# Kernel optimization log

Hardware: AMD Instinct MI355X
Metric: run time of the kernel (lower is better)

Reference implementation:

```python
import jax, jax.numpy as jnp
import numpy as np

# Hyperparameters (from init_kwargs)
D_MODEL = 1024
D_STATE = 64
HEADDIM = 64
MIMO_RANK = 2
CHUNK = 128
EXPAND = 2
D_INNER = EXPAND * D_MODEL            # 2048
NHEADS = D_INNER // HEADDIM           # 32
G = MIMO_RANK * D_STATE               # effective state channels per head = 128
D_CONV = 4
D_XBC = D_INNER + 2 * NHEADS * G      # conv channels
D_IN_PROJ = 2 * D_INNER + 2 * NHEADS * G + NHEADS  # [z, x, B, C, dt]


def rmsnorm(x, w, eps=1e-5):
    return x * w * jax.lax.rsqrt(jnp.mean(x * x, axis=-1, keepdims=True) + eps)


def setup_inputs() -> dict:
    key = jax.random.key(0)
    ks = jax.random.split(key, 8)
    B, L = 2, 2048
    x = jax.random.normal(ks[0], (B, L, D_MODEL), jnp.float32)
    norm_w = jnp.ones((D_MODEL,), jnp.float32)
    in_proj_w = jax.random.normal(ks[1], (D_IN_PROJ, D_MODEL), jnp.float32) * 0.02
    conv_w = jax.random.normal(ks[2], (D_XBC, D_CONV), jnp.float32) * 0.2
    conv_b = jnp.zeros((D_XBC,), jnp.float32)
    dt_bias = jax.random.uniform(ks[3], (NHEADS,), jnp.float32, minval=-4.0, maxval=-1.0)
    A_log = jnp.log(jax.random.uniform(ks[4], (NHEADS,), jnp.float32, minval=1.0, maxval=8.0))
    D_skip = jnp.ones((NHEADS,), jnp.float32)
    gnorm_w = jnp.ones((D_INNER,), jnp.float32)
    out_proj_w = jax.random.normal(ks[5], (D_MODEL, D_INNER), jnp.float32) * 0.02
    return dict(x=x, norm_w=norm_w, in_proj_w=in_proj_w, conv_w=conv_w, conv_b=conv_b,
                dt_bias=dt_bias, A_log=A_log, D_skip=D_skip, gnorm_w=gnorm_w,
                out_proj_w=out_proj_w)


def _mamba3(u, in_proj_w, conv_w, conv_b, dt_bias, A_log, D_skip, gnorm_w, out_proj_w):
    B, L, _ = u.shape
    H, P = NHEADS, HEADDIM
    nc = L // CHUNK

    zxbcdt = u @ in_proj_w.T                                   # (B,L,D_IN_PROJ)
    z, xbc, dt_raw = jnp.split(zxbcdt, [D_INNER, D_INNER + D_XBC], axis=-1)

    # causal depthwise conv (width D_CONV) + SiLU on [x, B, C]
    xp = jnp.pad(xbc, ((0, 0), (D_CONV - 1, 0), (0, 0)))
    conv = conv_b + sum(xp[:, k:k + L, :] * conv_w[:, k] for k in range(D_CONV))
    xbc = jax.nn.silu(conv)
    xh, Bm, Cm = jnp.split(xbc, [D_INNER, D_INNER + H * G], axis=-1)

    Xc = xh.reshape(B, nc, CHUNK, H, P)
    Bc = Bm.reshape(B, nc, CHUNK, H, G)
    Cc = Cm.reshape(B, nc, CHUNK, H, G)

    dt = jax.nn.softplus(dt_raw + dt_bias)                     # (B,L,H), positive
    A = -jnp.exp(A_log)                                        # (H,), negative
    dtc = dt.reshape(B, nc, CHUNK, H)
    a = dtc * A                                                # log decay, (B,nc,cs,H)
    cum = jnp.cumsum(a, axis=2)                                # inclusive cumsum within chunk

    # intra-chunk (quadratic, causal) part
    cumT = cum.transpose(0, 1, 3, 2)                           # (B,nc,H,cs)
    diff = cumT[..., :, None] - cumT[..., None, :]             # cum_l - cum_s
    mask = jnp.tril(jnp.ones((CHUNK, CHUNK), bool))
    decay = jnp.where(mask, jnp.exp(jnp.where(mask, diff, 0.0)), 0.0)
    dtT = dtc.transpose(0, 1, 3, 2)                            # (B,nc,H,cs)
    scores = jnp.einsum('bclhg,bcshg->bchls', Cc, Bc) * decay * dtT[:, :, :, None, :]
    Y_intra = jnp.einsum('bchls,bcshp->bclhp', scores, Xc)

    # inter-chunk state recurrence
    w = jnp.exp(cum[:, :, -1:, :] - cum) * dtc                 # (B,nc,cs,H)
    S = jnp.einsum('bcshg,bcshp->bchgp', Bc * w[..., None], Xc)  # chunk states
    dlast = jnp.exp(cum[:, :, -1, :])                          # (B,nc,H) total chunk decay

    def step(carry, inp):
        dl, s = inp
        return dl[:, :, None, None] * carry + s, carry

    init = jnp.zeros((B, H, G, P), u.dtype)
    _, Hprev = jax.lax.scan(step, init, (dlast.transpose(1, 0, 2), S.transpose(1, 0, 2, 3, 4)))
    Hprev = Hprev.transpose(1, 0, 2, 3, 4)                     # (B,nc,H,G,P) state before chunk
    Y_inter = jnp.einsum('bclhg,bchgp->bclhp', Cc * jnp.exp(cum)[..., None], Hprev)

    y = (Y_intra + Y_inter + D_skip[:, None] * Xc).reshape(B, L, D_INNER)
    y = rmsnorm(y * jax.nn.silu(z), gnorm_w)                   # gated RMSNorm
    return y @ out_proj_w.T


def reference(x, norm_w, in_proj_w, conv_w, conv_b, dt_bias, A_log, D_skip, gnorm_w, out_proj_w):
    # pre-norm residual wrapper
    return x + _mamba3(rmsnorm(x, norm_w), in_proj_w, conv_w, conv_b,
                       dt_bias, A_log, D_skip, gnorm_w, out_proj_w)
```

## Files before the change

kernel.cpp:

```cpp
#include <hip/hip_runtime.h>

typedef unsigned short u16;
typedef __attribute__((ext_vector_type(8))) short bf16x8;
typedef __attribute__((ext_vector_type(4))) float f32x4;

#define MFMA16(a,b,c) __builtin_amdgcn_mfma_f32_16x16x32_bf16(a,b,c,0,0,0)

#define DMODEL   1024
#define DINNER   2048
#define NHEADS   32
#define HEADDIM  64
#define GDIM     128
#define DXBC     10240
#define DPROJ    12320
#define CHUNK_L  128
#define NCHUNK   16
#define NROWS    4096

__device__ __forceinline__ float b2f(u16 u){ return __uint_as_float(((unsigned)u)<<16); }
__device__ __forceinline__ u16 f2b(float f){
  unsigned u = __float_as_uint(f);
  u += 0x7fffu + ((u>>16)&1u);
  return (u16)(u>>16);
}

__device__ __forceinline__ void gload_lds16(const void* g, void* l){
  __builtin_amdgcn_global_load_lds(
      (const __attribute__((address_space(1))) unsigned int*)g,
      (__attribute__((address_space(3))) unsigned int*)l, 16, 0, 0);
}

__global__ void k_f32_to_bf16(const float* __restrict__ src, u16* __restrict__ dst, int n){
  int i = blockIdx.x*blockDim.x + threadIdx.x;
  int stride = gridDim.x*blockDim.x;
  int n4 = n >> 2;
  for (int j=i; j<n4; j+=stride){
    float4 v = reinterpret_cast<const float4*>(src)[j];
    uint2 o;
    o.x = (unsigned)f2b(v.x) | ((unsigned)f2b(v.y)<<16);
    o.y = (unsigned)f2b(v.z) | ((unsigned)f2b(v.w)<<16);
    reinterpret_cast<uint2*>(dst)[j] = o;
  }
}

__global__ __launch_bounds__(256) void k_rmsnorm_in(const float* __restrict__ x,
                                                    const float* __restrict__ w,
                                                    u16* __restrict__ u){
  int row = blockIdx.x, tid = threadIdx.x;
  float4 v = reinterpret_cast<const float4*>(x + (size_t)row*DMODEL)[tid];
  float ss = v.x*v.x + v.y*v.y + v.z*v.z + v.w*v.w;
  #pragma unroll
  for (int off=32; off>0; off>>=1) ss += __shfl_down(ss, off, 64);
  __shared__ float red[4];
  if ((tid&63)==0) red[tid>>6] = ss;
  __syncthreads();
  float tot = red[0]+red[1]+red[2]+red[3];
  float sc = rsqrtf(tot/(float)DMODEL + 1e-5f);
  float4 wv = reinterpret_cast<const float4*>(w)[tid];
  uint2 o;
  o.x = (unsigned)f2b(v.x*wv.x*sc) | ((unsigned)f2b(v.y*wv.y*sc)<<16);
  o.y = (unsigned)f2b(v.z*wv.z*sc) | ((unsigned)f2b(v.w*wv.w*sc)<<16);
  reinterpret_cast<uint2*>(u + (size_t)row*DMODEL)[tid] = o;
}

__global__ __launch_bounds__(512) void k_gemm1_p2(const u16* __restrict__ A,
                                                  const u16* __restrict__ W,
                                                  u16* __restrict__ zb,
                                                  u16* __restrict__ xbc){
  __shared__ __align__(16) u16 lds[2*16384];
  const int tid  = threadIdx.x;
  const int lane = tid & 63, w = tid >> 6;
  const int wr = w >> 2, wc = w & 3;
  int bid = blockIdx.x;
  int xcd = bid & 7, g = bid >> 3;
  int st  = xcd*6 + (g >> 4);
  int wi  = g & 15;
  int tm  = (st/12)*4 + (wi>>2);
  int tn  = (st%12)*4 + (wi&3);
  const int m0 = tm*256, n0 = tn*256;

  const int srcslot = ((lane&3) ^ ((lane>>3)&3)) * 8;
  const u16* aS0 = A + (size_t)(m0 + w*16 + (lane>>2))*DMODEL + srcslot;
  const u16* aS1 = aS0 + (size_t)128*DMODEL;
  const u16* bS0 = W + (size_t)(n0 + w*16 + (lane>>2))*DMODEL + srcslot;
  const u16* bS1 = bS0 + (size_t)128*DMODEL;
  const int ldsW = (w*16)*32;
  const int rr = lane & 15;
  const int kb = (((lane>>4) ^ ((lane>>1)&3))) * 8;

  f32x4 acc[8][4];
  #pragma unroll
  for (int i=0;i<8;i++)
    #pragma unroll
    for (int j=0;j<4;j++) acc[i][j] = (f32x4){0,0,0,0};

  int stage_off = 0;
  auto STAGE = [&](int kt){
    u16* base = lds + (kt&1)*16384;
    gload_lds16(aS0 + stage_off, base + ldsW);
    gload_lds16(aS1 + stage_off, base + 128*32 + ldsW);
    gload_lds16(bS0 + stage_off, base + 8192 + ldsW);
    gload_lds16(bS1 + stage_off, base + 8192 + 128*32 + ldsW);
    stage_off += 32;
  };

  auto KTILE = [&](int kt, int stage_kt){
    const u16* As = lds + (kt&1)*16384;
    const u16* Bs = As + 8192;
    bf16x8 bf[4], af0[4], af1[4];
    #pragma unroll
    for (int tj=0;tj<4;tj++)
      bf[tj] = *(const bf16x8*)&Bs[(wc*64 + tj*16 + rr)*32 + kb];
    #pragma unroll
    for (int ti=0;ti<4;ti++)
      af0[ti] = *(const bf16x8*)&As[(wr*128 + ti*16 + rr)*32 + kb];
    __builtin_amdgcn_s_setprio(1);
    #pragma unroll
    for (int ti=0;ti<4;ti++)
      #pragma unroll
      for (int tj=0;tj<4;tj++)
        acc[ti][tj] = MFMA16(af0[ti], bf[tj], acc[ti][tj]);
    __builtin_amdgcn_s_setprio(0);
    #pragma unroll
    for (int ti=0;ti<4;ti++)
      af1[ti] = *(const bf16x8*)&As[(wr*128 + 64 + ti*16 + rr)*32 + kb];
    asm volatile("s_waitcnt lgkmcnt(0)" ::: "memory");
    __builtin_amdgcn_s_barrier();
    if (stage_kt >= 0) STAGE(stage_kt);
    __builtin_amdgcn_s_setprio(1);
    #pragma unroll
    for (int ti=0;ti<4;ti++)
      #pragma unroll
      for (int tj=0;tj<4;tj++)
        acc[4+ti][tj] = MFMA16(af1[ti], bf[tj], acc[4+ti][tj]);
    __builtin_amdgcn_s_setprio(0);
  };

  STAGE(0); STAGE(1);
  asm volatile("s_waitcnt vmcnt(4)" ::: "memory");
  __builtin_amdgcn_s_barrier();
  __builtin_amdgcn_sched_barrier(0);

  for (int kt = 0; kt < 30; ++kt){
    KTILE(kt, kt+2);
    asm volatile("s_waitcnt vmcnt(4)" ::: "memory");
    __builtin_amdgcn_s_barrier();
    __builtin_amdgcn_sched_barrier(0);
  }
  KTILE(30, -1);
  asm volatile("s_waitcnt vmcnt(0)" ::: "memory");
  __builtin_amdgcn_s_barrier();
  __builtin_amdgcn_sched_barrier(0);
  KTILE(31, -1);

  const int row0 = m0 + wr*128 + (lane>>4)*4;
  const int colb = wc*64 + (lane&15);
  if (tn >= 8){
    const int cb = n0 - DINNER;
    #pragma unroll
    for (int ti=0;ti<8;ti++)
      #pragma unroll
      for (int tj=0;tj<4;tj++)
        #pragma unroll
        for (int q=0;q<4;q++)
          xbc[(size_t)(row0 + ti*16 + q)*DXBC + cb + colb + tj*16] = f2b(acc[ti][tj][q]);
  } else {
    #pragma unroll
    for (int ti=0;ti<8;ti++)
      #pragma unroll
      for (int tj=0;tj<4;tj++)
        #pragma unroll
        for (int q=0;q<4;q++)
          zb[(size_t)(row0 + ti*16 + q)*DINNER + n0 + colb + tj*16] = f2b(acc[ti][tj][q]);
  }
}

__global__ __launch_bounds__(256) void k_gemm_dt(const u16* __restrict__ A,
                                                 const u16* __restrict__ W,
                                                 float* __restrict__ dtraw){
  const int lane = threadIdx.x & 63, wv = threadIdx.x >> 6;
  const int m0 = blockIdx.x*32;
  const int n0 = DINNER + DXBC;
  const int r  = lane & 15;
  const int kb = (lane>>4)*8;
  const int k0 = wv*256;
  const u16* a0p = A + (size_t)(m0 + r)*DMODEL + k0 + kb;
  const u16* a1p = a0p + 16*DMODEL;
  const u16* b0p = W + (size_t)(n0 + r)*DMODEL + k0 + kb;
  const u16* b1p = b0p + 16*DMODEL;
  f32x4 acc00={0,0,0,0}, acc01={0,0,0,0}, acc10={0,0,0,0}, acc11={0,0,0,0};
  #pragma unroll
  for (int k=0;k<256;k+=32){
    bf16x8 a0 = *(const bf16x8*)(a0p + k);
    bf16x8 a1 = *(const bf16x8*)(a1p + k);
    bf16x8 b0 = *(const bf16x8*)(b0p + k);
    bf16x8 b1 = *(const bf16x8*)(b1p + k);
    acc00 = MFMA16(a0,b0,acc00);
    acc01 = MFMA16(a0,b1,acc01);
    acc10 = MFMA16(a1,b0,acc10);
    acc11 = MFMA16(a1,b1,acc11);
  }
  __shared__ float part[4][1024];
  int rowb = (lane>>4)*4, col = lane&15;
  #pragma unroll
  for (int rr=0; rr<4; rr++){
    part[wv][(rowb+rr)*32 + col]         = acc00[rr];
    part[wv][(rowb+rr)*32 + col+16]      = acc01[rr];
    part[wv][(rowb+16+rr)*32 + col]      = acc10[rr];
    part[wv][(rowb+16+rr)*32 + col+16]   = acc11[rr];
  }
  __syncthreads();
  int idx = threadIdx.x*4;
  #pragma unroll
  for (int q=0;q<4;q++){
    int i = idx+q;
    dtraw[(size_t)m0*NHEADS + i] = part[0][i]+part[1][i]+part[2][i]+part[3][i];
  }
}

__global__ __launch_bounds__(256) void k_conv(const u16* __restrict__ xbc,
                                              const float* __restrict__ cw,
                                              const float* __restrict__ cb,
                                              u16* __restrict__ xh,
                                              u16* __restrict__ Bm,
                                              u16* __restrict__ Cm){
  int c  = (blockIdx.x*256 + threadIdx.x)*2;
  int row0 = blockIdx.y*8;
  int l0 = row0 & 2047;
  float4 wa = reinterpret_cast<const float4*>(cw)[c];
  float4 wb = reinterpret_cast<const float4*>(cw)[c+1];
  float cba = cb[c], cbb = cb[c+1];
  float a3=0,a2=0,a1=0, b3=0,b2=0,b1=0;
  auto loadpair = [&](int rw, float& fa, float& fb){
    unsigned v = *(const unsigned*)&xbc[(size_t)rw*DXBC + c];
    fa = b2f((u16)v); fb = b2f((u16)(v>>16));
  };
  if (l0 >= 3){
    loadpair(row0-3, a3,b3); loadpair(row0-2, a2,b2); loadpair(row0-1, a1,b1);
  }
  #pragma unroll
  for (int i=0;i<8;i++){
    float a0,b0; loadpair(row0+i, a0,b0);
    float sa = cba + a3*wa.x + a2*wa.y + a1*wa.z + a0*wa.w;
    float sb = cbb + b3*wb.x + b2*wb.y + b1*wb.z + b0*wb.w;
    sa = sa/(1.f+expf(-sa)); sb = sb/(1.f+expf(-sb));
    unsigned o = (unsigned)f2b(sa) | ((unsigned)f2b(sb)<<16);
    int rw = row0 + i;
    if (c < DINNER)            *(unsigned*)&xh[(size_t)rw*DINNER + c] = o;
    else if (c < DINNER+4096)  *(unsigned*)&Bm[(size_t)rw*4096 + (c-DINNER)] = o;
    else                       *(unsigned*)&Cm[(size_t)rw*4096 + (c-DINNER-4096)] = o;
    a3=a2; a2=a1; a1=a0; b3=b2; b2=b1; b1=b0;
  }
}

__global__ __launch_bounds__(128) void k_dtscan(const float* __restrict__ dtraw,
                                                const float* __restrict__ dt_bias,
                                                const float* __restrict__ A_log,
                                                float* __restrict__ dtT,
                                                float* __restrict__ cumT){
  int blk = blockIdx.x;
  int h   = blk & 31;
  int bc  = blk >> 5;
  int s   = threadIdx.x;
  int row = bc*128 + s;
  float xv = dtraw[(size_t)row*NHEADS + h] + dt_bias[h];
  float dt = (xv > 20.f) ? xv : log1pf(expf(xv));
  float a  = dt * (-expf(A_log[h]));
  __shared__ float lds[128];
  lds[s] = a; __syncthreads();
  #pragma unroll
  for (int off=1; off<128; off<<=1){
    float t = (s>=off) ? lds[s-off] : 0.f;
    __syncthreads();
    lds[s] += t;
    __syncthreads();
  }
  dtT[(size_t)blk*128 + s]  = dt;
  cumT[(size_t)blk*128 + s] = lds[s];
}

__global__ __launch_bounds__(256) void k_states(const u16* __restrict__ Bm,
                                                const u16* __restrict__ xh,
                                                const float* __restrict__ dtT,
                                                const float* __restrict__ cumT,
                                                float* __restrict__ S){
  int blk = blockIdx.x;
  int h = blk & 31, bc = blk >> 5;
  __shared__ __align__(16) u16 Bw[128][136];
  __shared__ __align__(16) u16 XT[64][136];
  __shared__ float cum[128], dtv[128];
  int tid = threadIdx.x;
  if (tid < 128){ cum[tid] = cumT[(size_t)blk*128+tid]; dtv[tid] = dtT[(size_t)blk*128+tid]; }
  __syncthreads();
  float clast = cum[127];
  for (int i = tid; i < 128*128; i += 256){
    int s = i >> 7, g = i & 127;
    float w = expf(clast - cum[s]) * dtv[s];
    Bw[g][s] = f2b(b2f(Bm[(size_t)(bc*128+s)*4096 + h*128 + g]) * w);
  }
  for (int i = tid; i < 64*128; i += 256){
    int s = i >> 6, p = i & 63;
    XT[p][s] = xh[(size_t)(bc*128+s)*DINNER + h*64 + p];
  }
  __syncthreads();
  int lane = tid & 63, wv = tid >> 6;
  int r = lane & 15, kb = (lane>>4)*8;
  f32x4 acc[2][4];
  #pragma unroll
  for (int i=0;i<2;i++)
    #pragma unroll
    for (int j=0;j<4;j++) acc[i][j] = (f32x4){0,0,0,0};
  #pragma unroll
  for (int k=0;k<128;k+=32){
    bf16x8 a0 = *(const bf16x8*)&Bw[wv*32 + r][k+kb];
    bf16x8 a1 = *(const bf16x8*)&Bw[wv*32 + 16 + r][k+kb];
    #pragma unroll
    for (int tj=0;tj<4;tj++){
      bf16x8 bb = *(const bf16x8*)&XT[tj*16 + r][k+kb];
      acc[0][tj] = MFMA16(a0,bb,acc[0][tj]);
      acc[1][tj] = MFMA16(a1,bb,acc[1][tj]);
    }
  }
  float* Sp = S + (size_t)blk*8192;
  int g0 = wv*32 + (lane>>4)*4, p0 = lane&15;
  #pragma unroll
  for (int ti=0;ti<2;ti++)
    #pragma unroll
    for (int tj=0;tj<4;tj++)
      #pragma unroll
      for (int rr=0;rr<4;rr++)
        Sp[(g0 + ti*16 + rr)*64 + tj*16 + p0] = acc[ti][tj][rr];
}

__global__ __launch_bounds__(256) void k_scan(const float* __restrict__ S,
                                              const float* __restrict__ cumT,
                                              u16* __restrict__ Hp){
  int slice = blockIdx.x & 7;
  int bh = blockIdx.x >> 3;
  int b = bh >> 5, h = bh & 31;
  int e0 = slice*1024 + threadIdx.x*4;
  float4 carry = {0,0,0,0};
  for (int c=0;c<NCHUNK;c++){
    int blk = (b*16+c)*32 + h;
    float dl = expf(cumT[(size_t)blk*128 + 127]);
    float4 s = *(const float4*)&S[(size_t)blk*8192 + e0];
    uint2 o;
    o.x = (unsigned)f2b(carry.x) | ((unsigned)f2b(carry.y)<<16);
    o.y = (unsigned)f2b(carry.z) | ((unsigned)f2b(carry.w)<<16);
    *reinterpret_cast<uint2*>(&Hp[(size_t)blk*8192 + e0]) = o;
    carry.x = dl*carry.x + s.x;
    carry.y = dl*carry.y + s.y;
    carry.z = dl*carry.z + s.z;
    carry.w = dl*carry.w + s.w;
  }
}

__global__ __launch_bounds__(256) void k_intra(const u16* __restrict__ Cm,
                                               const u16* __restrict__ Bm,
                                               const u16* __restrict__ xh,
                                               const u16* __restrict__ Hp,
                                               const float* __restrict__ dtT,
                                               const float* __restrict__ cumT,
                                               const float* __restrict__ Dskip,
                                               u16* __restrict__ yh){
  int blk = blockIdx.x;
  int h = blk & 31, bc = blk >> 5;
  __shared__ __align__(16) u16 Cl[128][136];
  __shared__ __align__(16) u16 Bl[128][136];
  __shared__ __align__(16) u16 XT[64][136];
  __shared__ __align__(16) u16 HT[64][136];
  __shared__ float cum[128], dtv[128];
  int tid = threadIdx.x;
  if (tid < 128){ cum[tid] = cumT[(size_t)blk*128+tid]; dtv[tid] = dtT[(size_t)blk*128+tid]; }
  for (int i = tid; i < 128*128; i += 256){
    int rw = i >> 7, g = i & 127;
    Cl[rw][g] = Cm[(size_t)(bc*128+rw)*4096 + h*128 + g];
    Bl[rw][g] = Bm[(size_t)(bc*128+rw)*4096 + h*128 + g];
  }
  for (int i = tid; i < 64*128; i += 256){
    int s = i >> 6, p = i & 63;
    XT[p][s] = xh[(size_t)(bc*128+s)*DINNER + h*64 + p];
  }
  for (int i = tid; i < 64*128; i += 256){
    int g = i >> 6, p = i & 63;
    HT[p][g] = Hp[(size_t)blk*8192 + g*64 + p];
  }
  __syncthreads();
  int lane = tid & 63, wv = tid >> 6;
  int r = lane & 15, kb = (lane>>4)*8;

  f32x4 p1[2][8];
  #pragma unroll
  for (int i=0;i<2;i++)
    #pragma unroll
    for (int j=0;j<8;j++) p1[i][j] = (f32x4){0,0,0,0};
  #pragma unroll
  for (int k=0;k<128;k+=32){
    bf16x8 a0 = *(const bf16x8*)&Cl[wv*32 + r][k+kb];
    bf16x8 a1 = *(const bf16x8*)&Cl[wv*32 + 16 + r][k+kb];
    #pragma unroll
    for (int tj=0;tj<8;tj++){
      bf16x8 bb = *(const bf16x8*)&Bl[tj*16 + r][k+kb];
      p1[0][tj] = MFMA16(a0,bb,p1[0][tj]);
      p1[1][tj] = MFMA16(a1,bb,p1[1][tj]);
    }
  }
  __syncthreads();
  int row0 = wv*32 + (lane>>4)*4;
  #pragma unroll
  for (int ti=0;ti<2;ti++)
    #pragma unroll
    for (int tj=0;tj<8;tj++)
      #pragma unroll
      for (int rr=0;rr<4;rr++){
        int l = row0 + ti*16 + rr;
        int s = tj*16 + (lane&15);
        float v = p1[ti][tj][rr];
        v = (s <= l) ? v * expf(cum[l]-cum[s]) * dtv[s] : 0.f;
        Bl[l][s] = f2b(v);
      }
  __syncthreads();

  f32x4 y[2][4];
  #pragma unroll
  for (int i=0;i<2;i++)
    #pragma unroll
    for (int j=0;j<4;j++) y[i][j] = (f32x4){0,0,0,0};
  #pragma unroll
  for (int k=0;k<128;k+=32){
    bf16x8 a0 = *(const bf16x8*)&Cl[wv*32 + r][k+kb];
    bf16x8 a1 = *(const bf16x8*)&Cl[wv*32 + 16 + r][k+kb];
    #pragma unroll
    for (int tj=0;tj<4;tj++){
      bf16x8 bb = *(const bf16x8*)&HT[tj*16 + r][k+kb];
      y[0][tj] = MFMA16(a0,bb,y[0][tj]);
      y[1][tj] = MFMA16(a1,bb,y[1][tj]);
    }
  }
  #pragma unroll
  for (int ti=0;ti<2;ti++){
    #pragma unroll
    for (int rr=0;rr<4;rr++){
      float e = expf(cum[row0 + ti*16 + rr]);
      #pragma unroll
      for (int tj=0;tj<4;tj++) y[ti][tj][rr] *= e;
    }
  }
  #pragma unroll
  for (int k=0;k<128;k+=32){
    bf16x8 a0 = *(const bf16x8*)&Bl[wv*32 + r][k+kb];
    bf16x8 a1 = *(const bf16x8*)&Bl[wv*32 + 16 + r][k+kb];
    #pragma unroll
    for (int tj=0;tj<4;tj++){
      bf16x8 bb = *(const bf16x8*)&XT[tj*16 + r][k+kb];
      y[0][tj] = MFMA16(a0,bb,y[0][tj]);
      y[1][tj] = MFMA16(a1,bb,y[1][tj]);
    }
  }
  float Dh = Dskip[h];
  #pragma unroll
  for (int ti=0;ti<2;ti++)
    #pragma unroll
    for (int tj=0;tj<4;tj++)
      #pragma unroll
      for (int rr=0;rr<4;rr++){
        int l = row0 + ti*16 + rr;
        int p = tj*16 + (lane&15);
        float xv = b2f(XT[p][l]);
        yh[(size_t)(bc*128 + l)*DINNER + h*64 + p] = f2b(y[ti][tj][rr] + Dh*xv);
      }
}

__global__ __launch_bounds__(256) void k_gate(const u16* __restrict__ yh,
                                              const u16* __restrict__ zb,
                                              const float* __restrict__ gw,
                                              u16* __restrict__ out){
  int row = blockIdx.x, tid = threadIdx.x;
  const uint4 yv = reinterpret_cast<const uint4*>(yh + (size_t)row*DINNER)[tid];
  const uint4 zv = reinterpret_cast<const uint4*>(zb + (size_t)row*DINNER)[tid];
  const unsigned* yp = (const unsigned*)&yv;
  const unsigned* zp = (const unsigned*)&zv;
  float t[8]; float ss = 0.f;
  #pragma unroll
  for (int i=0;i<4;i++){
    float y0 = b2f((u16)yp[i]), y1 = b2f((u16)(yp[i]>>16));
    float z0 = b2f((u16)zp[i]), z1 = b2f((u16)(zp[i]>>16));
    float v0 = y0 * (z0 / (1.f + expf(-z0)));
    float v1 = y1 * (z1 / (1.f + expf(-z1)));
    t[2*i] = v0; t[2*i+1] = v1; ss += v0*v0 + v1*v1;
  }
  #pragma unroll
  for (int off=32; off>0; off>>=1) ss += __shfl_down(ss, off, 64);
  __shared__ float red[4];
  if ((tid&63)==0) red[tid>>6] = ss;
  __syncthreads();
  float tot = red[0]+red[1]+red[2]+red[3];
  float g = rsqrtf(tot/(float)DINNER + 1e-5f);
  const float4 g0 = reinterpret_cast<const float4*>(gw)[tid*2];
  const float4 g1 = reinterpret_cast<const float4*>(gw)[tid*2+1];
  uint4 o;
  unsigned* op = (unsigned*)&o;
  float gg[8] = {g0.x,g0.y,g0.z,g0.w,g1.x,g1.y,g1.z,g1.w};
  #pragma unroll
  for (int i=0;i<4;i++)
    op[i] = (unsigned)f2b(t[2*i]*gg[2*i]*g) | ((unsigned)f2b(t[2*i+1]*gg[2*i+1]*g)<<16);
  reinterpret_cast<uint4*>(out + (size_t)row*DINNER)[tid] = o;
}

__global__ __launch_bounds__(256) void k_gemm2_db(const u16* __restrict__ A,
                                                  const u16* __restrict__ W,
                                                  const float* __restrict__ xres,
                                                  float* __restrict__ out){
  __shared__ __align__(16) u16 lds[2*8192];
  const int tid  = threadIdx.x;
  const int lane = tid & 63, wv = tid >> 6;
  const int wr = wv >> 1, wc = wv & 1;
  const int NWG = 8*32, Q = NWG/8;
  int swz = (blockIdx.x & 7)*Q + (blockIdx.x >> 3);
  int tm = swz / 8, tn = swz % 8;
  int m0 = tm*128, n0 = tn*128;

  const int K = DINNER;
  const int srcslot = ((lane&3) ^ ((lane>>3)&3)) * 8;
  const u16* aS0 = A + (size_t)(m0 + wv*32 + (lane>>2))*K + srcslot;
  const u16* aS1 = aS0 + (size_t)16*K;
  const u16* bS0 = W + (size_t)(n0 + wv*32 + (lane>>2))*K + srcslot;
  const u16* bS1 = bS0 + (size_t)16*K;
  const int ldsW = (wv*32)*32;
  const int rr = lane & 15;
  const int kb = (((lane>>4) ^ ((lane>>1)&3))) * 8;

  f32x4 acc[4][4];
  #pragma unroll
  for (int i=0;i<4;i++)
    #pragma unroll
    for (int j=0;j<4;j++) acc[i][j] = (f32x4){0,0,0,0};

  int stage_off = 0;
  auto STAGE = [&](int ks){
    u16* base = lds + (ks&1)*8192;
    gload_lds16(aS0 + stage_off, base + ldsW);
    gload_lds16(aS1 + stage_off, base + 16*32 + ldsW);
    gload_lds16(bS0 + stage_off, base + 4096 + ldsW);
    gload_lds16(bS1 + stage_off, base + 4096 + 16*32 + ldsW);
    stage_off += 32;
  };
  auto KSTEP = [&](int ks, int stage_ks){
    const u16* As = lds + (ks&1)*8192;
    const u16* Bs = As + 4096;
    bf16x8 af[4], bw[4];
    #pragma unroll
    for (int t=0;t<4;t++){
      af[t] = *(const bf16x8*)&As[(wr*64 + t*16 + rr)*32 + kb];
      bw[t] = *(const bf16x8*)&Bs[(wc*64 + t*16 + rr)*32 + kb];
    }
    asm volatile("s_waitcnt lgkmcnt(0)" ::: "memory");
    __builtin_amdgcn_s_barrier();
    if (stage_ks >= 0) STAGE(stage_ks);
    __builtin_amdgcn_s_setprio(1);
    #pragma unroll
    for (int ti=0;ti<4;ti++)
      #pragma unroll
      for (int tj=0;tj<4;tj++)
        acc[ti][tj] = MFMA16(af[ti], bw[tj], acc[ti][tj]);
    __builtin_amdgcn_s_setprio(0);
  };

  STAGE(0); STAGE(1);
  asm volatile("s_waitcnt vmcnt(4)" ::: "memory");
  __builtin_amdgcn_s_barrier();
  __builtin_amdgcn_sched_barrier(0);
  const int NK = K/32;
  for (int ks = 0; ks < NK-2; ++ks){
    KSTEP(ks, ks+2);
    asm volatile("s_waitcnt vmcnt(4)" ::: "memory");
    __builtin_amdgcn_s_barrier();
    __builtin_amdgcn_sched_barrier(0);
  }
  KSTEP(NK-2, -1);
  asm volatile("s_waitcnt vmcnt(0)" ::: "memory");
  __builtin_amdgcn_s_barrier();
  __builtin_amdgcn_sched_barrier(0);
  KSTEP(NK-1, -1);

  int row0 = m0 + wr*64 + (lane>>4)*4;
  int col0 = n0 + wc*64 + (lane&15);
  #pragma unroll
  for (int ti=0;ti<4;ti++)
    #pragma unroll
    for (int tj=0;tj<4;tj++)
      #pragma unroll
      for (int q=0;q<4;q++){
        size_t idx = (size_t)(row0+ti*16+q)*DMODEL + col0 + tj*16;
        out[idx] = acc[ti][tj][q] + xres[idx];
      }
}

extern "C" void kernel_launch(void* const* d_in, const int* in_sizes, int n_in,
                              void* d_out, int out_size, void* d_ws, size_t ws_size,
                              hipStream_t stream) {
  (void)in_sizes; (void)n_in; (void)out_size; (void)ws_size;
  const float* x         = (const float*)d_in[0];
  const float* norm_w    = (const float*)d_in[1];
  const float* in_proj_w = (const float*)d_in[2];
  const float* conv_w    = (const float*)d_in[3];
  const float* conv_b    = (const float*)d_in[4];
  const float* dt_bias   = (const float*)d_in[5];
  const float* A_log     = (const float*)d_in[6];
  const float* D_skip    = (const float*)d_in[7];
  const float* gnorm_w   = (const float*)d_in[8];
  const float* out_proj_w= (const float*)d_in[9];
  float* out = (float*)d_out;

  char* ws = (char*)d_ws;
  size_t off = 0;
  auto alloc = [&](size_t bytes)->char*{
    char* p = ws + off; off = (off + bytes + 255) & ~(size_t)255; return p;
  };
  u16*   W2    = (u16*)  alloc((size_t)DMODEL*DINNER*2);
  u16*   zb    = (u16*)  alloc((size_t)NROWS*DINNER*2);
  float* dtraw = (float*)alloc((size_t)NROWS*NHEADS*4);
  float* dtT   = (float*)alloc((size_t)1024*128*4);
  float* cumT  = (float*)alloc((size_t)1024*128*4);
  u16*   xhb   = (u16*)  alloc((size_t)NROWS*DINNER*2);
  u16*   Bmb   = (u16*)  alloc((size_t)NROWS*4096*2);
  u16*   Cmb   = (u16*)  alloc((size_t)NROWS*4096*2);
  char*  R1    = alloc((size_t)NROWS*DXBC*2);
  u16*   xbcr  = (u16*)R1;
  float* S     = (float*)R1;
  u16*   Hp    = (u16*)(R1 + (size_t)1024*8192*4);
  u16*   yh    = (u16*)R1;
  char*  R2    = alloc((size_t)DPROJ*DMODEL*2 + (size_t)NROWS*DMODEL*2);
  u16*   W1    = (u16*)R2;
  u16*   u_bf  = (u16*)(R2 + (size_t)DPROJ*DMODEL*2);
  u16*   gated = (u16*)R2;

  k_f32_to_bf16<<<2048,256,0,stream>>>(in_proj_w, W1, DPROJ*DMODEL);
  k_f32_to_bf16<<<512,256,0,stream>>>(out_proj_w, W2, DMODEL*DINNER);
  k_rmsnorm_in<<<NROWS,256,0,stream>>>(x, norm_w, u_bf);
  k_gemm1_p2<<<768,512,0,stream>>>(u_bf, W1, zb, xbcr);
  k_gemm_dt<<<NROWS/32,256,0,stream>>>(u_bf, W1, dtraw);
  k_conv<<<dim3(DXBC/512, NROWS/8),256,0,stream>>>(xbcr, conv_w, conv_b, xhb, Bmb, Cmb);
  k_dtscan<<<1024,128,0,stream>>>(dtraw, dt_bias, A_log, dtT, cumT);
  k_states<<<1024,256,0,stream>>>(Bmb, xhb, dtT, cumT, S);
  k_scan<<<512,256,0,stream>>>(S, cumT, Hp);
  k_intra<<<1024,256,0,stream>>>(Cmb, Bmb, xhb, Hp, dtT, cumT, D_skip, yh);
  k_gate<<<NROWS,256,0,stream>>>(yh, zb, gnorm_w, gated);
  k_gemm2_db<<<8*32,256,0,stream>>>(gated, W2, x, out);
}
```

Before: 325.5 us.

## Restructure in-proj GEMM into 8-phase ping-pong pipeline with 64-wide K tiles

The in-projection GEMM now stages 64-wide K tiles (doubling LDS to 128KB across two buffers) and splits each K iteration into four MFMA quadrants. Global-to-LDS loads for the next tile are interleaved between quadrants, separated by barriers. An 8-way XOR swizzle replaces the 4-way one. The aim is to halve the number of K iterations and better overlap global loads with MFMA work. The cost is a large LDS footprint that limits occupancy, plus many more barriers.

```diff
diff --git a/kernel.cpp b/kernel.cpp
--- a/kernel.cpp
+++ b/kernel.cpp
@@ -63,11 +63,11 @@
   reinterpret_cast<uint2*>(u + (size_t)row*DMODEL)[tid] = o;
 }
 
-__global__ __launch_bounds__(512) void k_gemm1_p2(const u16* __restrict__ A,
+__global__ __launch_bounds__(512) void k_gemm1_8p(const u16* __restrict__ A,
                                                   const u16* __restrict__ W,
                                                   u16* __restrict__ zb,
                                                   u16* __restrict__ xbc){
-  __shared__ __align__(16) u16 lds[2*16384];
+  __shared__ __align__(16) u16 lds[65536];
   const int tid  = threadIdx.x;
   const int lane = tid & 63, w = tid >> 6;
   const int wr = w >> 2, wc = w & 3;
@@ -79,14 +79,13 @@
   int tn  = (st%12)*4 + (wi&3);
   const int m0 = tm*256, n0 = tn*256;
 
-  const int srcslot = ((lane&3) ^ ((lane>>3)&3)) * 8;
-  const u16* aS0 = A + (size_t)(m0 + w*16 + (lane>>2))*DMODEL + srcslot;
-  const u16* aS1 = aS0 + (size_t)128*DMODEL;
-  const u16* bS0 = W + (size_t)(n0 + w*16 + (lane>>2))*DMODEL + srcslot;
-  const u16* bS1 = bS0 + (size_t)128*DMODEL;
-  const int ldsW = (w*16)*32;
-  const int rr = lane & 15;
-  const int kb = (((lane>>4) ^ ((lane>>1)&3))) * 8;
+  const int srow = w*8 + (lane>>3);
+  const int scol = ((lane&7) ^ ((lane>>3)&7))*8;
+  const u16* aS = A + (size_t)(m0 + srow)*DMODEL + scol;
+  const u16* bS = W + (size_t)(n0 + srow)*DMODEL + scol;
+  const int ldsw = w*512;
+
+  const int rr = lane & 15, gq = lane >> 4;
 
   f32x4 acc[8][4];
   #pragma unroll
@@ -94,64 +93,110 @@
     #pragma unroll
     for (int j=0;j<4;j++) acc[i][j] = (f32x4){0,0,0,0};
 
-  int stage_off = 0;
-  auto STAGE = [&](int kt){
-    u16* base = lds + (kt&1)*16384;
-    gload_lds16(aS0 + stage_off, base + ldsW);
-    gload_lds16(aS1 + stage_off, base + 128*32 + ldsW);
-    gload_lds16(bS0 + stage_off, base + 8192 + ldsW);
-    gload_lds16(bS1 + stage_off, base + 8192 + 128*32 + ldsW);
-    stage_off += 32;
+  auto SU_A = [&](int kt, int j){
+    gload_lds16(aS + (size_t)(j*64)*DMODEL + kt*64,
+                lds + (kt&1)*32768 + j*4096 + ldsw);
   };
-
-  auto KTILE = [&](int kt, int stage_kt){
-    const u16* As = lds + (kt&1)*16384;
-    const u16* Bs = As + 8192;
-    bf16x8 bf[4], af0[4], af1[4];
-    #pragma unroll
-    for (int tj=0;tj<4;tj++)
-      bf[tj] = *(const bf16x8*)&Bs[(wc*64 + tj*16 + rr)*32 + kb];
-    #pragma unroll
-    for (int ti=0;ti<4;ti++)
-      af0[ti] = *(const bf16x8*)&As[(wr*128 + ti*16 + rr)*32 + kb];
-    __builtin_amdgcn_s_setprio(1);
-    #pragma unroll
-    for (int ti=0;ti<4;ti++)
-      #pragma unroll
-      for (int tj=0;tj<4;tj++)
-        acc[ti][tj] = MFMA16(af0[ti], bf[tj], acc[ti][tj]);
-    __builtin_amdgcn_s_setprio(0);
-    #pragma unroll
-    for (int ti=0;ti<4;ti++)
-      af1[ti] = *(const bf16x8*)&As[(wr*128 + 64 + ti*16 + rr)*32 + kb];
-    asm volatile("s_waitcnt lgkmcnt(0)" ::: "memory");
-    __builtin_amdgcn_s_barrier();
-    if (stage_kt >= 0) STAGE(stage_kt);
-    __builtin_amdgcn_s_setprio(1);
-    #pragma unroll
-    for (int ti=0;ti<4;ti++)
-      #pragma unroll
-      for (int tj=0;tj<4;tj++)
-        acc[4+ti][tj] = MFMA16(af1[ti], bf[tj], acc[4+ti][tj]);
-    __builtin_amdgcn_s_setprio(0);
+  auto SU_B = [&](int kt, int j){
+    gload_lds16(bS + (size_t)(j*64)*DMODEL + kt*64,
+                lds + (kt&1)*32768 + 16384 + j*4096 + ldsw);
   };
 
-  STAGE(0); STAGE(1);
-  asm volatile("s_waitcnt vmcnt(4)" ::: "memory");
+  SU_A(0,0); SU_A(0,2); SU_B(0,0); SU_B(0,2); SU_B(0,1); SU_B(0,3); SU_A(0,1); SU_A(0,3);
+  asm volatile("s_waitcnt vmcnt(2)" ::: "memory");
   __builtin_amdgcn_s_barrier();
   __builtin_amdgcn_sched_barrier(0);
 
-  for (int kt = 0; kt < 30; ++kt){
-    KTILE(kt, kt+2);
-    asm volatile("s_waitcnt vmcnt(4)" ::: "memory");
-    __builtin_amdgcn_s_barrier();
+  for (int kt = 0; kt < 16; ++kt){
+    const u16* bufA = lds + (kt&1)*32768;
+    const u16* bufB = bufA + 16384;
+    const bool stg = (kt < 15);
+    bf16x8 af[4][2], bw0[2][2], bw1[2][2];
+
+    auto RDA = [&](int ti, int ks)->bf16x8{
+      int r = wr*128 + ti*16 + rr;
+      int s = (ks*4 + gq) ^ (rr & 7);
+      return *(const bf16x8*)&bufA[r*64 + s*8];
+    };
+    auto RDB = [&](int tj, int ks)->bf16x8{
+      int r = wc*64 + tj*16 + rr;
+      int s = (ks*4 + gq) ^ (rr & 7);
+      return *(const bf16x8*)&bufB[r*64 + s*8];
+    };
+
+    #pragma unroll
+    for (int ti=0;ti<4;ti++){ af[ti][0]=RDA(ti,0); af[ti][1]=RDA(ti,1); }
+    #pragma unroll
+    for (int tj=0;tj<2;tj++){ bw0[tj][0]=RDB(tj,0); bw0[tj][1]=RDB(tj,1); }
+    if (stg){ SU_A(kt+1,0); SU_A(kt+1,2); }
+    __builtin_amdgcn_s_barrier();
+    asm volatile("s_waitcnt lgkmcnt(0)" ::: "memory");
     __builtin_amdgcn_sched_barrier(0);
-  }
-  KTILE(30, -1);
-  asm volatile("s_waitcnt vmcnt(0)" ::: "memory");
-  __builtin_amdgcn_s_barrier();
-  __builtin_amdgcn_sched_barrier(0);
-  KTILE(31, -1);
+    __builtin_amdgcn_s_setprio(1);
+    #pragma unroll
+    for (int ti=0;ti<4;ti++)
+      #pragma unroll
+      for (int tj=0;tj<2;tj++){
+        acc[ti][tj] = MFMA16(af[ti][0], bw0[tj][0], acc[ti][tj]);
+        acc[ti][tj] = MFMA16(af[ti][1], bw0[tj][1], acc[ti][tj]);
+      }
+    __builtin_amdgcn_s_setprio(0);
+    __builtin_amdgcn_s_barrier();
+
+    #pragma unroll
+    for (int tj=0;tj<2;tj++){ bw1[tj][0]=RDB(tj+2,0); bw1[tj][1]=RDB(tj+2,1); }
+    if (stg){ SU_B(kt+1,0); SU_B(kt+1,2); }
+    __builtin_amdgcn_s_barrier();
+    asm volatile("s_waitcnt lgkmcnt(0)" ::: "memory");
+    __builtin_amdgcn_sched_barrier(0);
+    __builtin_amdgcn_s_setprio(1);
+    #pragma unroll
+    for (int ti=0;ti<4;ti++)
+      #pragma unroll
+      for (int tj=0;tj<2;tj++){
+        acc[ti][tj+2] = MFMA16(af[ti][0], bw1[tj][0], acc[ti][tj+2]);
+        acc[ti][tj+2] = MFMA16(af[ti][1], bw1[tj][1], acc[ti][tj+2]);
+      }
+    __builtin_amdgcn_s_setprio(0);
+    if (stg) asm volatile("s_waitcnt vmcnt(4)" ::: "memory");
+    else     asm volatile("s_waitcnt vmcnt(0)" ::: "memory");
+    __builtin_amdgcn_s_barrier();
+
+    #pragma unroll
+    for (int ti=0;ti<4;ti++){ af[ti][0]=RDA(ti+4,0); af[ti][1]=RDA(ti+4,1); }
+    if (stg){ SU_B(kt+1,1); SU_B(kt+1,3); }
+    __builtin_amdgcn_s_barrier();
+    asm volatile("s_waitcnt lgkmcnt(0)" ::: "memory");
+    __builtin_amdgcn_sched_barrier(0);
+    __builtin_amdgcn_s_setprio(1);
+    #pragma unroll
+    for (int ti=0;ti<4;ti++)
+      #pragma unroll
+      for (int tj=0;tj<2;tj++){
+        acc[4+ti][tj] = MFMA16(af[ti][0], bw0[tj][0], acc[4+ti][tj]);
+        acc[4+ti][tj] = MFMA16(af[ti][1], bw0[tj][1], acc[4+ti][tj]);
+      }
+    __builtin_amdgcn_s_setprio(0);
+    __builtin_amdgcn_s_barrier();
+
+    if (stg){ SU_A(kt+1,1); SU_A(kt+1,3); }
+    __builtin_amdgcn_s_barrier();
+    __builtin_amdgcn_sched_barrier(0);
+    __builtin_amdgcn_s_setprio(1);
+    #pragma unroll
+    for (int ti=0;ti<4;ti++)
+      #pragma unroll
+      for (int tj=0;tj<2;tj++){
+        acc[4+ti][tj+2] = MFMA16(af[ti][0], bw1[tj][0], acc[4+ti][tj+2]);
+        acc[4+ti][tj+2] = MFMA16(af[ti][1], bw1[tj][1], acc[4+ti][tj+2]);
+      }
+    __builtin_amdgcn_s_setprio(0);
+    if (stg){
+      asm volatile("s_waitcnt vmcnt(2)" ::: "memory");
+      __builtin_amdgcn_s_barrier();
+      __builtin_amdgcn_sched_barrier(0);
+    }
+  }
 
   const int row0 = m0 + wr*128 + (lane>>4)*4;
   const int colb = wc*64 + (lane&15);
@@ -638,7 +683,7 @@
   k_f32_to_bf16<<<2048,256,0,stream>>>(in_proj_w, W1, DPROJ*DMODEL);
   k_f32_to_bf16<<<512,256,0,stream>>>(out_proj_w, W2, DMODEL*DINNER);
   k_rmsnorm_in<<<NROWS,256,0,stream>>>(x, norm_w, u_bf);
-  k_gemm1_p2<<<768,512,0,stream>>>(u_bf, W1, zb, xbcr);
+  k_gemm1_8p<<<768,512,0,stream>>>(u_bf, W1, zb, xbcr);
   k_gemm_dt<<<NROWS/32,256,0,stream>>>(u_bf, W1, dtraw);
   k_conv<<<dim3(DXBC/512, NROWS/8),256,0,stream>>>(xbcr, conv_w, conv_b, xhb, Bmb, Cmb);
   k_dtscan<<<1024,128,0,stream>>>(dtraw, dt_bias, A_log, dtT, cumT);
```

Measured after the change: 317.1 us. 2.6% less time.
